# Optimization experiments

Measured on AMD Instinct MI355X. Metric: run time of the kernel, lower is better.

The kernel has to match this reference:

```python
import jax, jax.numpy as jnp
import numpy as np
import math

B, S, HID = 2, 2048, 2048
NH, HD = 16, HID // 16          # num_heads, head_dim
RING = 4
CH = S // RING                  # chunk size per ring rank
SEG_LEN = 2048                  # segment_lengths[0]
DIL = 2                         # dilation_rates[0]


def setup_inputs() -> dict:
    key = jax.random.key(0)
    k1, k2, k3 = jax.random.split(key, 3)
    x = jax.random.normal(k1, (B, S, HID), dtype=jnp.float32)
    # Linear weights stored input-major so y = x @ W (same math as torch x @ W.T)
    W_qkv = jax.random.normal(k2, (HID, 3 * HID), dtype=jnp.float32) * 0.02
    W_out = jax.random.normal(k3, (HID, HID), dtype=jnp.float32) * 0.02
    return {"x": x, "W_qkv": W_qkv, "W_out": W_out}


def _dilated_mask():
    # mask[i, j] = (segment(i) == segment(j)) and (|i - j| % DIL == 0)
    pos = jnp.arange(S)
    seg = pos // SEG_LEN
    same_seg = seg[:, None] == seg[None, :]
    dil_ok = (jnp.abs(pos[:, None] - pos[None, :]) % DIL) == 0
    return same_seg & dil_ok  # [S, S] bool


def reference(x, W_qkv, W_out):
    qkv = (x @ W_qkv).reshape(B, S, 3, NH, HD)
    q, k, v = jnp.moveaxis(qkv, 2, 0)          # each [B, S, NH, HD]
    q = jnp.transpose(q, (0, 2, 1, 3))          # [B, NH, S, HD]
    k = jnp.transpose(k, (0, 2, 1, 3))
    v = jnp.transpose(v, (0, 2, 1, 3))

    scores = jnp.einsum('bhqd,bhkd->bhqk', q, k) / math.sqrt(HD)  # [B,NH,S,S]
    if DIL > 1:
        scores = jnp.where(_dilated_mask()[None, None], scores, -jnp.inf)

    # Reshape into (q-chunk, kv-chunk) blocks to reproduce the per-chunk
    # (non-rescaled) softmax of the ring loop: each kv chunk subtracts its OWN
    # max, exps, and the un-rescaled numerators/denominators are summed.
    s = scores.reshape(B, NH, RING, CH, RING, CH)        # [B,H,Rq,Cq,Rk,Ck]
    m = jnp.max(s, axis=-1, keepdims=True)               # per-kv-chunk row max
    e = jnp.exp(s - m)                                   # -inf -> 0
    v_ch = v.reshape(B, NH, RING, CH, HD)                # [B,H,Rk,Ck,HD]
    num = jnp.einsum('bhqcrk,bhrkd->bhqcd', e, v_ch)     # [B,H,Rq,Cq,HD]
    den = jnp.sum(e, axis=(-2, -1))[..., None]           # [B,H,Rq,Cq,1]
    out = num / (den + 1e-8)

    out = out.reshape(B, NH, S, HD)
    out = jnp.transpose(out, (0, 2, 1, 3)).reshape(B, S, HID)
    return out @ W_out
```

## Files before the change

### kernel.cpp

```cpp
#include <hip/hip_runtime.h>
#include <stdint.h>

typedef float  f32x4  __attribute__((ext_vector_type(4)));
typedef __bf16 bf16x8 __attribute__((ext_vector_type(8)));

#define AS1 __attribute__((address_space(1)))
#define AS3 __attribute__((address_space(3)))


__global__ void k_cvt_x_blk(const float* __restrict__ x, __bf16* __restrict__ y) {
  const int d = blockIdx.x * 256 + threadIdx.x;
  const int row = d & 127, kg = (d >> 7) & 3, mbkt = d >> 9;
  const int mb = mbkt & 31, kt = mbkt >> 5;
  const int m = mb * 128 + row, k0 = kt * 32 + kg * 8;
  const float4 v0 = *reinterpret_cast<const float4*>(x + (size_t)m * 2048 + k0);
  const float4 v1 = *reinterpret_cast<const float4*>(x + (size_t)m * 2048 + k0 + 4);
  bf16x8 o;
  o[0] = (__bf16)v0.x; o[1] = (__bf16)v0.y; o[2] = (__bf16)v0.z; o[3] = (__bf16)v0.w;
  o[4] = (__bf16)v1.x; o[5] = (__bf16)v1.y; o[6] = (__bf16)v1.z; o[7] = (__bf16)v1.w;
  *reinterpret_cast<bf16x8*>(y + (size_t)d * 8) = o;
}

__global__ void k_cvt_wt(const float* __restrict__ w, __bf16* __restrict__ wt,
                         const int K, const int N) {
  __shared__ float tile[64][65];
  const int k0 = blockIdx.x * 64, n0 = blockIdx.y * 64;
  const int t = threadIdx.x;
  #pragma unroll
  for (int i = 0; i < 16; ++i) {
    const int idx = t + 256 * i;
    const int r = idx >> 6, c = idx & 63;
    tile[r][c] = w[(size_t)(k0 + r) * N + n0 + c];
  }
  __syncthreads();
  #pragma unroll
  for (int i = 0; i < 16; ++i) {
    const int idx = t + 256 * i;
    const int r = idx >> 6, c = idx & 63;
    wt[(size_t)(n0 + r) * K + k0 + c] = (__bf16)tile[c][r];
  }
}

__global__ void k_cvt_wt_blk(const float* __restrict__ w, __bf16* __restrict__ wt,
                             const int N, const int NBK) {
  __shared__ float tile[64][65];
  const int k0 = blockIdx.x * 64, n0 = blockIdx.y * 64;
  const int t = threadIdx.x;
  #pragma unroll
  for (int i = 0; i < 16; ++i) {
    const int idx = t + 256 * i;
    const int r = idx >> 6, c = idx & 63;
    tile[r][c] = w[(size_t)(k0 + r) * N + n0 + c];
  }
  __syncthreads();
  #pragma unroll
  for (int i = 0; i < 16; ++i) {
    const int idx = t + 256 * i;
    const int nn = idx >> 6, kk = idx & 63;
    const int n = n0 + nn, k = k0 + kk;
    const size_t dst = ((size_t)(k >> 5) * NBK + (n >> 7)) * 4096 +
                       (size_t)((k >> 3) & 3) * 1024 + (n & 127) * 8 + (k & 7);
    wt[dst] = (__bf16)tile[kk][nn];
  }
}

__global__ __launch_bounds__(256, 3) void k_gemm1p(
    const __bf16* __restrict__ Ab, const __bf16* __restrict__ Bb,
    __bf16* __restrict__ Oq, __bf16* __restrict__ Ok, __bf16* __restrict__ Ov) {
  __shared__ __bf16 As[3][4096];
  __shared__ __bf16 Bs[3][4096];
  const int tid = threadIdx.x;
  const int w = tid >> 6, l = tid & 63, g = l >> 4, l15 = l & 15;
  const int wr = w >> 1, wc = w & 1;
  const int bx = blockIdx.x;
  const int wid = (bx & 7) * 192 + (bx >> 3);
  const int nb = wid % 48, mb = wid / 48;
  const size_t Abase = (size_t)mb * 4096, Bbase = (size_t)nb * 4096;
  const size_t Astep = 32 * 4096, Bstep = 48 * 4096;
  const int soff = w * 1024;

  f32x4 acc[4][4] = {};

  auto STAGE = [&](int t, int b) {
    const __bf16* as_ = Ab + (size_t)t * Astep + Abase + soff + l * 8;
    const __bf16* bs_ = Bb + (size_t)t * Bstep + Bbase + soff + l * 8;
    __builtin_amdgcn_global_load_lds((const AS1 uint32_t*)as_,
                                     (AS3 uint32_t*)(&As[b][soff]), 16, 0, 0);
    __builtin_amdgcn_global_load_lds((const AS1 uint32_t*)(as_ + 512),
                                     (AS3 uint32_t*)(&As[b][soff + 512]), 16, 0, 0);
    __builtin_amdgcn_global_load_lds((const AS1 uint32_t*)bs_,
                                     (AS3 uint32_t*)(&Bs[b][soff]), 16, 0, 0);
    __builtin_amdgcn_global_load_lds((const AS1 uint32_t*)(bs_ + 512),
                                     (AS3 uint32_t*)(&Bs[b][soff + 512]), 16, 0, 0);
  };

  STAGE(0, 0);
  STAGE(1, 1);
  asm volatile("s_waitcnt vmcnt(4)" ::: "memory");
  __builtin_amdgcn_s_barrier();

  int cur = 0;
  for (int t = 0; t < 64; ++t) {
    int b2 = cur + 2; if (b2 >= 3) b2 -= 3;
    if (t + 2 < 64) STAGE(t + 2, b2);
    const __bf16* Ar = &As[cur][g * 1024 + (wr * 64 + l15) * 8];
    const __bf16* Br = &Bs[cur][g * 1024 + (wc * 64 + l15) * 8];
    bf16x8 af[4], bfr[4];
    #pragma unroll
    for (int mi = 0; mi < 4; ++mi) af[mi] = *reinterpret_cast<const bf16x8*>(Ar + mi * 128);
    #pragma unroll
    for (int ni = 0; ni < 4; ++ni) bfr[ni] = *reinterpret_cast<const bf16x8*>(Br + ni * 128);
    __builtin_amdgcn_s_setprio(1);
    #pragma unroll
    for (int mi = 0; mi < 4; ++mi)
      #pragma unroll
      for (int ni = 0; ni < 4; ++ni)
        acc[mi][ni] = __builtin_amdgcn_mfma_f32_16x16x32_bf16(af[mi], bfr[ni], acc[mi][ni], 0, 0, 0);
    __builtin_amdgcn_s_setprio(0);
    __builtin_amdgcn_sched_barrier(0);
    if (t < 62) asm volatile("s_waitcnt vmcnt(4)" ::: "memory");
    else        asm volatile("s_waitcnt vmcnt(0)" ::: "memory");
    __builtin_amdgcn_s_barrier();
    cur = cur + 1; if (cur >= 3) cur -= 3;
  }

  const int m0 = mb * 128, n0 = nb * 128;
  const int ty = n0 >> 11;
  const int h = (n0 & 2047) >> 7;
  #pragma unroll
  for (int mi = 0; mi < 4; ++mi) {
    #pragma unroll
    for (int r = 0; r < 4; ++r) {
      const int m = m0 + wr * 64 + mi * 16 + 4 * g + r;
      const int s = m & 2047;
      const int sp = s & 1, s2 = s >> 1;
      const int bb = m >> 11;
      const size_t base = ((((size_t)bb * 16 + h) * 2 + sp) << 17);
      #pragma unroll
      for (int ni = 0; ni < 4; ++ni) {
        const int d = wc * 64 + ni * 16 + l15;
        const __bf16 v = (__bf16)acc[mi][ni][r];
        if (ty == 0)      Oq[base + (size_t)s2 * 128 + d] = v;
        else if (ty == 1) Ok[base + (size_t)s2 * 128 + d] = v;
        else              Ov[base + (size_t)d * 1024 + s2] = v;
      }
    }
  }
}

__global__ __launch_bounds__(256, 2) void k_gemm_bt2(
    const __bf16* __restrict__ A, const __bf16* __restrict__ Bt,
    float* __restrict__ Of, const int M, const int N, const int K) {
  __shared__ __bf16 As[128 * 32];
  __shared__ __bf16 Bs[128 * 32];
  const int tid = threadIdx.x;
  const int w = tid >> 6, l = tid & 63, g = l >> 4, l15 = l & 15;
  const int wr = w >> 1, wc = w & 1;
  const int m0 = blockIdx.y * 128, n0 = blockIdx.x * 128;
  const int srow = l >> 2, scol = (l & 3) * 8;

  f32x4 acc[4][4] = {};

  for (int kt = 0; kt < K; kt += 32) {
    __syncthreads();
    #pragma unroll
    for (int i = 0; i < 2; ++i) {
      const int ch = w * 2 + i;
      const int row = ch * 16 + srow;
      __builtin_amdgcn_global_load_lds(
          (const AS1 uint32_t*)(A + (size_t)(m0 + row) * K + kt + scol),
          (AS3 uint32_t*)(As + ch * 512), 16, 0, 0);
      __builtin_amdgcn_global_load_lds(
          (const AS1 uint32_t*)(Bt + (size_t)(n0 + row) * K + kt + scol),
          (AS3 uint32_t*)(Bs + ch * 512), 16, 0, 0);
    }
    __syncthreads();

    bf16x8 af[4], bfr[4];
    #pragma unroll
    for (int mi = 0; mi < 4; ++mi)
      af[mi] = *reinterpret_cast<const bf16x8*>(As + (wr * 64 + mi * 16 + l15) * 32 + 8 * g);
    #pragma unroll
    for (int ni = 0; ni < 4; ++ni)
      bfr[ni] = *reinterpret_cast<const bf16x8*>(Bs + (wc * 64 + ni * 16 + l15) * 32 + 8 * g);
    #pragma unroll
    for (int mi = 0; mi < 4; ++mi)
      #pragma unroll
      for (int ni = 0; ni < 4; ++ni)
        acc[mi][ni] = __builtin_amdgcn_mfma_f32_16x16x32_bf16(af[mi], bfr[ni], acc[mi][ni], 0, 0, 0);
  }

  #pragma unroll
  for (int mi = 0; mi < 4; ++mi)
    #pragma unroll
    for (int ni = 0; ni < 4; ++ni)
      #pragma unroll
      for (int r = 0; r < 4; ++r) {
        const int m = m0 + wr * 64 + mi * 16 + 4 * g + r;
        const int n = n0 + wc * 64 + ni * 16 + l15;
        Of[(size_t)m * N + n] = acc[mi][ni][r];
      }
}

__global__ __launch_bounds__(256, 2) void k_attn(
    const __bf16* __restrict__ Qp, const __bf16* __restrict__ Kp,
    const __bf16* __restrict__ Vt, __bf16* __restrict__ attn) {
  __shared__ __bf16 Ks[64 * 128];
  __shared__ __bf16 Vs[128 * 64];
  __shared__ __bf16 E[4][16][136];

  const int bx = blockIdx.x;
  const int wid = (bx & 7) * 128 + (bx >> 3);
  const int qt = wid & 15, p = (wid >> 4) & 1, h = (wid >> 5) & 15, b = wid >> 9;
  const int tid = threadIdx.x;
  const int w = tid >> 6, l = tid & 63, g = l >> 4, l15 = l & 15;
  const size_t base = ((((size_t)b * 16 + h) * 2 + p) << 17);
  const __bf16* Qb = Qp + base;
  const __bf16* Kb = Kp + base;
  const __bf16* Vb = Vt + base;
  const int q0 = qt * 64 + w * 16;
  const float SC = 1.4426950408889634f / 11.313708498984761f;

  bf16x8 qf[4];
  #pragma unroll
  for (int ks = 0; ks < 4; ++ks)
    qf[ks] = *reinterpret_cast<const bf16x8*>(Qb + (size_t)(q0 + l15) * 128 + ks * 32 + 8 * g);

  f32x4 num[8] = {};
  float den[4] = {0.f, 0.f, 0.f, 0.f};

  const int krow_in = l >> 4;
  const int vrow_in = l >> 3;
  const int vsrc_e = (((l & 7) * 16) ^ (vrow_in << 4)) >> 1;

  for (int c = 0; c < 4; ++c) {
    f32x4 s[16] = {};
    #pragma unroll
    for (int st = 0; st < 4; ++st) {
      __syncthreads();
      #pragma unroll
      for (int i = 0; i < 4; ++i) {
        const int ch = w * 4 + i;
        const int row = ch * 4 + krow_in;
        const int cb = (l15 * 16) ^ ((row & 7) << 4);
        const __bf16* src = Kb + (size_t)(c * 256 + st * 64 + row) * 128 + (cb >> 1);
        __builtin_amdgcn_global_load_lds((const AS1 uint32_t*)src,
                                         (AS3 uint32_t*)(Ks + ch * 512), 16, 0, 0);
      }
      __syncthreads();
      #pragma unroll
      for (int ks = 0; ks < 4; ++ks) {
        #pragma unroll
        for (int nf2 = 0; nf2 < 4; ++nf2) {
          const int r = nf2 * 16 + l15;
          const int cb = (ks * 64 + g * 16) ^ ((r & 7) << 4);
          const bf16x8 kf = *reinterpret_cast<const bf16x8*>(Ks + r * 128 + (cb >> 1));
          s[st * 4 + nf2] = __builtin_amdgcn_mfma_f32_16x16x32_bf16(qf[ks], kf, s[st * 4 + nf2], 0, 0, 0);
        }
      }
    }
    float mv[4];
    #pragma unroll
    for (int r = 0; r < 4; ++r) {
      float m0v = s[0][r];
      #pragma unroll
      for (int nf = 1; nf < 16; ++nf) m0v = fmaxf(m0v, s[nf][r]);
      m0v = fmaxf(m0v, __shfl_xor(m0v, 1));
      m0v = fmaxf(m0v, __shfl_xor(m0v, 2));
      m0v = fmaxf(m0v, __shfl_xor(m0v, 4));
      m0v = fmaxf(m0v, __shfl_xor(m0v, 8));
      mv[r] = m0v;
    }
    #pragma unroll
    for (int r = 0; r < 4; ++r) {
      float ds = 0.f;
      #pragma unroll
      for (int nf = 0; nf < 16; ++nf) {
        const float e = exp2f((s[nf][r] - mv[r]) * SC);
        s[nf][r] = e;
        ds += e;
      }
      den[r] += ds;
    }
    #pragma unroll
    for (int h2 = 0; h2 < 2; ++h2) {
      #pragma unroll
      for (int nf = 0; nf < 8; ++nf)
        #pragma unroll
        for (int r = 0; r < 4; ++r)
          E[w][4 * g + r][nf * 16 + l15] = (__bf16)s[h2 * 8 + nf][r];
      #pragma unroll
      for (int sv = 0; sv < 2; ++sv) {
        const int kv0 = c * 256 + h2 * 128 + sv * 64;
        __syncthreads();
        #pragma unroll
        for (int i = 0; i < 4; ++i) {
          const int ch = w * 4 + i;
          const int row = ch * 8 + vrow_in;
          const __bf16* src = Vb + (size_t)row * 1024 + kv0 + vsrc_e;
          __builtin_amdgcn_global_load_lds((const AS1 uint32_t*)src,
                                           (AS3 uint32_t*)(Vs + ch * 512), 16, 0, 0);
        }
        __syncthreads();
        #pragma unroll
        for (int ks2 = 0; ks2 < 2; ++ks2) {
          const bf16x8 a = *reinterpret_cast<const bf16x8*>(
              &E[w][l15][sv * 64 + ks2 * 32 + 8 * g]);
          #pragma unroll
          for (int nd = 0; nd < 8; ++nd) {
            const int d = nd * 16 + l15;
            const int cb = (ks2 * 64 + g * 16) ^ ((d & 7) << 4);
            const bf16x8 vf = *reinterpret_cast<const bf16x8*>(Vs + d * 64 + (cb >> 1));
            num[nd] = __builtin_amdgcn_mfma_f32_16x16x32_bf16(a, vf, num[nd], 0, 0, 0);
          }
        }
      }
    }
  }

  #pragma unroll
  for (int r = 0; r < 4; ++r) {
    den[r] += __shfl_xor(den[r], 1);
    den[r] += __shfl_xor(den[r], 2);
    den[r] += __shfl_xor(den[r], 4);
    den[r] += __shfl_xor(den[r], 8);
    den[r] += 1e-8f;
  }

  #pragma unroll
  for (int nd = 0; nd < 8; ++nd)
    #pragma unroll
    for (int r = 0; r < 4; ++r) {
      const int sq = q0 + 4 * g + r;
      const int srow = 2 * sq + p;
      attn[((size_t)b * 2048 + srow) * 2048 + h * 128 + nd * 16 + l15] =
          (__bf16)(num[nd][r] / den[r]);
    }
}

extern "C" void kernel_launch(void* const* d_in, const int* in_sizes, int n_in,
                              void* d_out, int out_size, void* d_ws, size_t ws_size,
                              hipStream_t stream) {
  (void)in_sizes; (void)n_in; (void)out_size; (void)ws_size;
  const float* x    = (const float*)d_in[0];
  const float* wqkv = (const float*)d_in[1];
  const float* wout = (const float*)d_in[2];
  float* out = (float*)d_out;
  uint8_t* ws = (uint8_t*)d_ws;

  __bf16* xbf   = (__bf16*)(ws + 0);
  __bf16* wqkvt = (__bf16*)(ws + (16ull << 20));
  __bf16* woutt = (__bf16*)(ws + (40ull << 20));
  __bf16* Qp    = (__bf16*)(ws + (48ull << 20));
  __bf16* Kp    = (__bf16*)(ws + (64ull << 20));
  __bf16* Vt    = (__bf16*)(ws + (80ull << 20));
  __bf16* attn  = (__bf16*)(ws + 0);

  k_cvt_x_blk<<<4096, 256, 0, stream>>>(x, xbf);
  k_cvt_wt_blk<<<dim3(32, 96), 256, 0, stream>>>(wqkv, wqkvt, 6144, 48);
  k_cvt_wt<<<dim3(32, 32), 256, 0, stream>>>(wout, woutt, 2048, 2048);
  k_gemm1p<<<1536, 256, 0, stream>>>(xbf, wqkvt, Qp, Kp, Vt);
  k_attn<<<1024, 256, 0, stream>>>(Qp, Kp, Vt, attn);
  k_gemm_bt2<<<dim3(16, 32), 256, 0, stream>>>(attn, woutt, out, 4096, 2048, 2048);
}
```

Before: 285.8 us.

## Unify GEMMs into pipelined 128x256 blocked-layout kernel and pre-block attention output

Replaces the QKV GEMM and the output-projection GEMM with one templated kernel that uses 128x256 tiles (4x8 MFMA accumulators per wave) and a 3-stage global_load_lds pipeline. The attention kernel now writes its output directly in the pre-blocked layout, and W_out is converted with the blocked converter, so the second GEMM can use the same contiguous staging as the first instead of a synchronous row-major loader. Larger tiles improve operand reuse, but they raise register and LDS pressure, cut occupancy to 2 blocks per CU, and give the output GEMM only 256 blocks, which may underfill the GPU.

```diff
diff --git a/kernel.cpp b/kernel.cpp
--- a/kernel.cpp
+++ b/kernel.cpp
@@ -21,26 +21,6 @@
   *reinterpret_cast<bf16x8*>(y + (size_t)d * 8) = o;
 }
 
-__global__ void k_cvt_wt(const float* __restrict__ w, __bf16* __restrict__ wt,
-                         const int K, const int N) {
-  __shared__ float tile[64][65];
-  const int k0 = blockIdx.x * 64, n0 = blockIdx.y * 64;
-  const int t = threadIdx.x;
-  #pragma unroll
-  for (int i = 0; i < 16; ++i) {
-    const int idx = t + 256 * i;
-    const int r = idx >> 6, c = idx & 63;
-    tile[r][c] = w[(size_t)(k0 + r) * N + n0 + c];
-  }
-  __syncthreads();
-  #pragma unroll
-  for (int i = 0; i < 16; ++i) {
-    const int idx = t + 256 * i;
-    const int r = idx >> 6, c = idx & 63;
-    wt[(size_t)(n0 + r) * K + k0 + c] = (__bf16)tile[c][r];
-  }
-}
-
 __global__ void k_cvt_wt_blk(const float* __restrict__ w, __bf16* __restrict__ wt,
                              const int N, const int NBK) {
   __shared__ float tile[64][65];
@@ -64,147 +44,112 @@
   }
 }
 
-__global__ __launch_bounds__(256, 3) void k_gemm1p(
+template<int NBB, int NBX, int EPI>
+__global__ __launch_bounds__(256, 2) void k_gemm_blk(
     const __bf16* __restrict__ Ab, const __bf16* __restrict__ Bb,
-    __bf16* __restrict__ Oq, __bf16* __restrict__ Ok, __bf16* __restrict__ Ov) {
+    __bf16* __restrict__ Oq, __bf16* __restrict__ Ok, __bf16* __restrict__ Ov,
+    float* __restrict__ Of) {
   __shared__ __bf16 As[3][4096];
-  __shared__ __bf16 Bs[3][4096];
+  __shared__ __bf16 Bs[3][8192];
   const int tid = threadIdx.x;
   const int w = tid >> 6, l = tid & 63, g = l >> 4, l15 = l & 15;
-  const int wr = w >> 1, wc = w & 1;
+  const int wq = w >> 1, wc = w & 1;
   const int bx = blockIdx.x;
-  const int wid = (bx & 7) * 192 + (bx >> 3);
-  const int nb = wid % 48, mb = wid / 48;
-  const size_t Abase = (size_t)mb * 4096, Bbase = (size_t)nb * 4096;
-  const size_t Astep = 32 * 4096, Bstep = 48 * 4096;
-  const int soff = w * 1024;
-
-  f32x4 acc[4][4] = {};
+  const int xcd = bx & 7, win = bx >> 3;
+  const int nb = xcd * NBX + win / 32;
+  const int mb = win % 32;
+
+  f32x4 acc[4][8] = {};
 
   auto STAGE = [&](int t, int b) {
-    const __bf16* as_ = Ab + (size_t)t * Astep + Abase + soff + l * 8;
-    const __bf16* bs_ = Bb + (size_t)t * Bstep + Bbase + soff + l * 8;
-    __builtin_amdgcn_global_load_lds((const AS1 uint32_t*)as_,
-                                     (AS3 uint32_t*)(&As[b][soff]), 16, 0, 0);
-    __builtin_amdgcn_global_load_lds((const AS1 uint32_t*)(as_ + 512),
-                                     (AS3 uint32_t*)(&As[b][soff + 512]), 16, 0, 0);
-    __builtin_amdgcn_global_load_lds((const AS1 uint32_t*)bs_,
-                                     (AS3 uint32_t*)(&Bs[b][soff]), 16, 0, 0);
-    __builtin_amdgcn_global_load_lds((const AS1 uint32_t*)(bs_ + 512),
-                                     (AS3 uint32_t*)(&Bs[b][soff + 512]), 16, 0, 0);
+    const __bf16* abase = Ab + ((size_t)t * 32 + mb) * 4096;
+    #pragma unroll
+    for (int i = 0; i < 2; ++i) {
+      const int ch = w * 2 + i;
+      __builtin_amdgcn_global_load_lds((const AS1 uint32_t*)(abase + ch * 512 + l * 8),
+                                       (AS3 uint32_t*)(&As[b][ch * 512]), 16, 0, 0);
+    }
+    const __bf16* bbase = Bb + ((size_t)t * NBB + nb * 2) * 4096;
+    #pragma unroll
+    for (int i = 0; i < 4; ++i) {
+      const int cb = w * 4 + i;
+      __builtin_amdgcn_global_load_lds((const AS1 uint32_t*)(bbase + cb * 512 + l * 8),
+                                       (AS3 uint32_t*)(&Bs[b][cb * 512]), 16, 0, 0);
+    }
   };
 
   STAGE(0, 0);
   STAGE(1, 1);
-  asm volatile("s_waitcnt vmcnt(4)" ::: "memory");
+  asm volatile("s_waitcnt vmcnt(6)" ::: "memory");
   __builtin_amdgcn_s_barrier();
 
   int cur = 0;
   for (int t = 0; t < 64; ++t) {
     int b2 = cur + 2; if (b2 >= 3) b2 -= 3;
     if (t + 2 < 64) STAGE(t + 2, b2);
-    const __bf16* Ar = &As[cur][g * 1024 + (wr * 64 + l15) * 8];
-    const __bf16* Br = &Bs[cur][g * 1024 + (wc * 64 + l15) * 8];
-    bf16x8 af[4], bfr[4];
-    #pragma unroll
-    for (int mi = 0; mi < 4; ++mi) af[mi] = *reinterpret_cast<const bf16x8*>(Ar + mi * 128);
-    #pragma unroll
-    for (int ni = 0; ni < 4; ++ni) bfr[ni] = *reinterpret_cast<const bf16x8*>(Br + ni * 128);
+    bf16x8 af[4], bfr[8];
+    #pragma unroll
+    for (int mi = 0; mi < 4; ++mi)
+      af[mi] = *reinterpret_cast<const bf16x8*>(
+          &As[cur][g * 1024 + (wq * 64 + mi * 16 + l15) * 8]);
+    #pragma unroll
+    for (int ni = 0; ni < 8; ++ni)
+      bfr[ni] = *reinterpret_cast<const bf16x8*>(
+          &Bs[cur][wc * 4096 + g * 1024 + (ni * 16 + l15) * 8]);
     __builtin_amdgcn_s_setprio(1);
     #pragma unroll
     for (int mi = 0; mi < 4; ++mi)
       #pragma unroll
-      for (int ni = 0; ni < 4; ++ni)
+      for (int ni = 0; ni < 8; ++ni)
         acc[mi][ni] = __builtin_amdgcn_mfma_f32_16x16x32_bf16(af[mi], bfr[ni], acc[mi][ni], 0, 0, 0);
     __builtin_amdgcn_s_setprio(0);
-    __builtin_amdgcn_sched_barrier(0);
-    if (t < 62) asm volatile("s_waitcnt vmcnt(4)" ::: "memory");
+    if (t < 62) asm volatile("s_waitcnt vmcnt(6)" ::: "memory");
     else        asm volatile("s_waitcnt vmcnt(0)" ::: "memory");
     __builtin_amdgcn_s_barrier();
     cur = cur + 1; if (cur >= 3) cur -= 3;
   }
 
-  const int m0 = mb * 128, n0 = nb * 128;
-  const int ty = n0 >> 11;
-  const int h = (n0 & 2047) >> 7;
-  #pragma unroll
-  for (int mi = 0; mi < 4; ++mi) {
-    #pragma unroll
-    for (int r = 0; r < 4; ++r) {
-      const int m = m0 + wr * 64 + mi * 16 + 4 * g + r;
-      const int s = m & 2047;
-      const int sp = s & 1, s2 = s >> 1;
-      const int bb = m >> 11;
-      const size_t base = ((((size_t)bb * 16 + h) * 2 + sp) << 17);
-      #pragma unroll
-      for (int ni = 0; ni < 4; ++ni) {
-        const int d = wc * 64 + ni * 16 + l15;
-        const __bf16 v = (__bf16)acc[mi][ni][r];
-        if (ty == 0)      Oq[base + (size_t)s2 * 128 + d] = v;
-        else if (ty == 1) Ok[base + (size_t)s2 * 128 + d] = v;
-        else              Ov[base + (size_t)d * 1024 + s2] = v;
-      }
-    }
-  }
-}
-
-__global__ __launch_bounds__(256, 2) void k_gemm_bt2(
-    const __bf16* __restrict__ A, const __bf16* __restrict__ Bt,
-    float* __restrict__ Of, const int M, const int N, const int K) {
-  __shared__ __bf16 As[128 * 32];
-  __shared__ __bf16 Bs[128 * 32];
-  const int tid = threadIdx.x;
-  const int w = tid >> 6, l = tid & 63, g = l >> 4, l15 = l & 15;
-  const int wr = w >> 1, wc = w & 1;
-  const int m0 = blockIdx.y * 128, n0 = blockIdx.x * 128;
-  const int srow = l >> 2, scol = (l & 3) * 8;
-
-  f32x4 acc[4][4] = {};
-
-  for (int kt = 0; kt < K; kt += 32) {
-    __syncthreads();
-    #pragma unroll
-    for (int i = 0; i < 2; ++i) {
-      const int ch = w * 2 + i;
-      const int row = ch * 16 + srow;
-      __builtin_amdgcn_global_load_lds(
-          (const AS1 uint32_t*)(A + (size_t)(m0 + row) * K + kt + scol),
-          (AS3 uint32_t*)(As + ch * 512), 16, 0, 0);
-      __builtin_amdgcn_global_load_lds(
-          (const AS1 uint32_t*)(Bt + (size_t)(n0 + row) * K + kt + scol),
-          (AS3 uint32_t*)(Bs + ch * 512), 16, 0, 0);
-    }
-    __syncthreads();
-
-    bf16x8 af[4], bfr[4];
+  if constexpr (EPI == 1) {
+    const int n0 = nb * 256 + wc * 128;
+    const int ty = n0 >> 11;
+    const int h = (n0 & 2047) >> 7;
+    #pragma unroll
+    for (int mi = 0; mi < 4; ++mi) {
+      #pragma unroll
+      for (int r = 0; r < 4; ++r) {
+        const int m = mb * 128 + wq * 64 + mi * 16 + 4 * g + r;
+        const int s = m & 2047;
+        const int sp = s & 1, s2 = s >> 1;
+        const int bb = m >> 11;
+        const size_t base = ((((size_t)bb * 16 + h) * 2 + sp) << 17);
+        #pragma unroll
+        for (int ni = 0; ni < 8; ++ni) {
+          const int d = ni * 16 + l15;
+          const __bf16 v = (__bf16)acc[mi][ni][r];
+          if (ty == 0)      Oq[base + (size_t)s2 * 128 + d] = v;
+          else if (ty == 1) Ok[base + (size_t)s2 * 128 + d] = v;
+          else              Ov[base + (size_t)d * 1024 + s2] = v;
+        }
+      }
+    }
+  } else {
     #pragma unroll
     for (int mi = 0; mi < 4; ++mi)
-      af[mi] = *reinterpret_cast<const bf16x8*>(As + (wr * 64 + mi * 16 + l15) * 32 + 8 * g);
-    #pragma unroll
-    for (int ni = 0; ni < 4; ++ni)
-      bfr[ni] = *reinterpret_cast<const bf16x8*>(Bs + (wc * 64 + ni * 16 + l15) * 32 + 8 * g);
-    #pragma unroll
-    for (int mi = 0; mi < 4; ++mi)
-      #pragma unroll
-      for (int ni = 0; ni < 4; ++ni)
-        acc[mi][ni] = __builtin_amdgcn_mfma_f32_16x16x32_bf16(af[mi], bfr[ni], acc[mi][ni], 0, 0, 0);
-  }
-
-  #pragma unroll
-  for (int mi = 0; mi < 4; ++mi)
-    #pragma unroll
-    for (int ni = 0; ni < 4; ++ni)
       #pragma unroll
       for (int r = 0; r < 4; ++r) {
-        const int m = m0 + wr * 64 + mi * 16 + 4 * g + r;
-        const int n = n0 + wc * 64 + ni * 16 + l15;
-        Of[(size_t)m * N + n] = acc[mi][ni][r];
-      }
+        const int m = mb * 128 + wq * 64 + mi * 16 + 4 * g + r;
+        #pragma unroll
+        for (int ni = 0; ni < 8; ++ni) {
+          const int n = nb * 256 + wc * 128 + ni * 16 + l15;
+          Of[(size_t)m * 2048 + n] = acc[mi][ni][r];
+        }
+      }
+  }
 }
 
 __global__ __launch_bounds__(256, 2) void k_attn(
     const __bf16* __restrict__ Qp, const __bf16* __restrict__ Kp,
-    const __bf16* __restrict__ Vt, __bf16* __restrict__ attn) {
+    const __bf16* __restrict__ Vt, __bf16* __restrict__ attnA) {
   __shared__ __bf16 Ks[64 * 128];
   __shared__ __bf16 Vs[128 * 64];
   __shared__ __bf16 E[4][16][136];
@@ -333,8 +278,11 @@
     for (int r = 0; r < 4; ++r) {
       const int sq = q0 + 4 * g + r;
       const int srow = 2 * sq + p;
-      attn[((size_t)b * 2048 + srow) * 2048 + h * 128 + nd * 16 + l15] =
-          (__bf16)(num[nd][r] / den[r]);
+      const int m = b * 2048 + srow;
+      const int k = h * 128 + nd * 16 + l15;
+      const size_t dst = ((size_t)(k >> 5) * 32 + (m >> 7)) * 4096 +
+                         (size_t)((k >> 3) & 3) * 1024 + (m & 127) * 8 + (k & 7);
+      attnA[dst] = (__bf16)(num[nd][r] / den[r]);
     }
 }
 
@@ -354,12 +302,12 @@
   __bf16* Qp    = (__bf16*)(ws + (48ull << 20));
   __bf16* Kp    = (__bf16*)(ws + (64ull << 20));
   __bf16* Vt    = (__bf16*)(ws + (80ull << 20));
-  __bf16* attn  = (__bf16*)(ws + 0);
+  __bf16* attnA = (__bf16*)(ws + 0);
 
   k_cvt_x_blk<<<4096, 256, 0, stream>>>(x, xbf);
   k_cvt_wt_blk<<<dim3(32, 96), 256, 0, stream>>>(wqkv, wqkvt, 6144, 48);
-  k_cvt_wt<<<dim3(32, 32), 256, 0, stream>>>(wout, woutt, 2048, 2048);
-  k_gemm1p<<<1536, 256, 0, stream>>>(xbf, wqkvt, Qp, Kp, Vt);
-  k_attn<<<1024, 256, 0, stream>>>(Qp, Kp, Vt, attn);
-  k_gemm_bt2<<<dim3(16, 32), 256, 0, stream>>>(attn, woutt, out, 4096, 2048, 2048);
-}
+  k_cvt_wt_blk<<<dim3(32, 32), 256, 0, stream>>>(wout, woutt, 2048, 16);
+  k_gemm_blk<48, 3, 1><<<768, 256, 0, stream>>>(xbf, wqkvt, Qp, Kp, Vt, nullptr);
+  k_attn<<<1024, 256, 0, stream>>>(Qp, Kp, Vt, attnA);
+  k_gemm_blk<16, 1, 2><<<256, 256, 0, stream>>>(attnA, woutt, nullptr, nullptr, nullptr, out);
+}
```

Result: slower. 344.3 us (+20.5%).
